# Performance work log

Hardware: AMD Instinct MI355X
Metric: run time of the kernel (lower is better)

## Reference

```python
import jax, jax.numpy as jnp
import numpy as np

TREND_SCALING = 0.6
DETAIL_PRESERVATION = 0.85
SPIKE_THRESHOLD = 3.5
SPIKE_DAMPING = 0.35
ITERATIONS = 2
EPS = 1e-6


def _smooth(x, kernel):
    # x: [B, C, L], kernel: [1, 1, W] (normalized box filter)
    W = kernel.shape[-1]
    pad = W // 2
    xp = jnp.pad(x, ((0, 0), (0, 0), (pad, pad)), mode='reflect')
    C = x.shape[1]
    w = jnp.broadcast_to(kernel, (C, 1, W))  # depthwise weight [C, 1, W]
    return jax.lax.conv_general_dilated(
        xp, w, window_strides=(1,), padding='VALID',
        dimension_numbers=('NCH', 'OIH', 'NCH'), feature_group_count=C)


def setup_inputs() -> dict:
    key = jax.random.key(0)
    x = jax.random.normal(key, (16, 32, 65536), dtype=jnp.float32)
    # buffers from __init__ with base_window=5
    detail_kernel = jnp.ones((1, 1, 5), dtype=jnp.float32) / 5.0
    trend_kernel = jnp.ones((1, 1, 11), dtype=jnp.float32) / 11.0
    return {"x": x, "detail_kernel": detail_kernel, "trend_kernel": trend_kernel}


def reference(x, detail_kernel, trend_kernel):
    current = x.astype(jnp.float32)
    for _ in range(ITERATIONS):
        trend = _smooth(current, trend_kernel)
        local = _smooth(current, detail_kernel)
        residual = current - local
        # torch .std uses Bessel's correction (ddof=1)
        scale = jnp.maximum(jnp.std(residual, axis=-1, keepdims=True, ddof=1), EPS)
        threshold = scale * SPIKE_THRESHOLD
        residual = jnp.where(jnp.abs(residual) > threshold,
                             residual * SPIKE_DAMPING, residual)
        residual = residual * DETAIL_PRESERVATION
        combined = (1.0 - TREND_SCALING) * local + TREND_SCALING * trend
        current = combined + residual
    return current
```

## Files before the change

kernel.cpp:

```cpp
#include <hip/hip_runtime.h>
#include <math.h>

#define LROW   65536
#define NROWS  512
#define CHUNK  4096
#define NCH    (LROW / CHUNK)
#define NT     256
#define EPT    (CHUNK / NT)
#define HALO   5
#define NELEM  (CHUNK + 2 * HALO)

#define TREND_SCALING       0.6f
#define DETAIL_PRESERVATION 0.85f
#define SPIKE_THRESHOLD     3.5f
#define SPIKE_DAMPING       0.35f
#define EPSV                1e-6f

#define PART_BYTES (NROWS * NCH * 2 * 8)

__device__ __forceinline__ int sw(int i) { return i + (i >> 4); }

template <bool STASH>
__global__ __launch_bounds__(NT) void k_sum(const float* __restrict__ src,
                                            const float* __restrict__ k5,
                                            double* __restrict__ partials,
                                            float* __restrict__ edges) {
    __shared__ float buf[NELEM + (NELEM >> 4) + 2];
    const int bid = blockIdx.x;
    const int row = bid >> 4;
    const int c = bid & (NCH - 1);
    const size_t rowBase = (size_t)row * LROW;
    const int cStart = c * CHUNK;
    const int tid = threadIdx.x;
    const float w5 = k5[0];

    const float4* src4 = (const float4*)(src + rowBase + cStart);
    for (int j4 = tid; j4 < CHUNK / 4; j4 += NT) {
        float4 t4 = src4[j4];
        int l = j4 * 4 + HALO;
        buf[sw(l)] = t4.x;
        buf[sw(l + 1)] = t4.y;
        buf[sw(l + 2)] = t4.z;
        buf[sw(l + 3)] = t4.w;
    }
    if (tid < 2 * HALO) {
        int j = (tid < HALO) ? tid : (CHUNK + tid);
        int g = cStart - HALO + j;
        g = (g < 0) ? -g : (g >= LROW ? 2 * LROW - 2 - g : g);
        buf[sw(j)] = src[rowBase + g];
    }
    __syncthreads();

    if (STASH && tid < 10) {
        int l = (tid < 5) ? (HALO + tid) : (CHUNK + tid - 5);
        edges[(size_t)bid * 10 + tid] = buf[sw(l)];
    }

    float v[EPT + 2 * HALO];
    const int base = tid * EPT;
#pragma unroll
    for (int j = 0; j < EPT + 2 * HALO; j++) v[j] = buf[sw(base + j)];

    double s = 0.0, q = 0.0;
#pragma unroll
    for (int k = 0; k < EPT; k++) {
        float lac = 0.f;
#pragma unroll
        for (int d = 0; d < 5; d++) lac = fmaf(v[k + 3 + d], w5, lac);
        float r = v[k + HALO] - lac;
        s += (double)r;
        q += (double)r * (double)r;
    }

    __shared__ double rs[NT], rq[NT];
    rs[tid] = s;
    rq[tid] = q;
    __syncthreads();
    for (int off = NT / 2; off > 0; off >>= 1) {
        if (tid < off) {
            rs[tid] += rs[tid + off];
            rq[tid] += rq[tid + off];
        }
        __syncthreads();
    }
    if (tid == 0) {
        partials[(size_t)bid * 2] = rs[0];
        partials[(size_t)bid * 2 + 1] = rq[0];
    }
}

__global__ void k_red(const double* __restrict__ partials, float* __restrict__ thr) {
    int r = blockIdx.x * blockDim.x + threadIdx.x;
    if (r >= NROWS) return;
    double s = 0.0, q = 0.0;
    for (int c = 0; c < NCH; c++) {
        s += partials[(size_t)(r * NCH + c) * 2];
        q += partials[(size_t)(r * NCH + c) * 2 + 1];
    }
    const double N = (double)LROW;
    double var = (q - s * s / N) / (N - 1.0);
    if (var < 0.0) var = 0.0;
    float sd = (float)sqrt(var);
    float scale = fmaxf(sd, EPSV);
    thr[r] = scale * SPIKE_THRESHOLD;
}

template <bool USE_EDGES>
__global__ __launch_bounds__(NT) void k_apply(const float* src, float* dst,
                                              const float* k5, const float* k11,
                                              const float* thr, const float* edges) {
    __shared__ float buf[NELEM + (NELEM >> 4) + 2];
    const int bid = blockIdx.x;
    const int row = bid >> 4;
    const int c = bid & (NCH - 1);
    const size_t rowBase = (size_t)row * LROW;
    const int cStart = c * CHUNK;
    const int tid = threadIdx.x;
    const float w5 = k5[0];
    const float w11 = k11[0];
    const float th = thr[row];

    const float4* src4 = (const float4*)(src + rowBase + cStart);
    for (int j4 = tid; j4 < CHUNK / 4; j4 += NT) {
        float4 t4 = src4[j4];
        int l = j4 * 4 + HALO;
        buf[sw(l)] = t4.x;
        buf[sw(l + 1)] = t4.y;
        buf[sw(l + 2)] = t4.z;
        buf[sw(l + 3)] = t4.w;
    }
    if (!USE_EDGES) {
        if (tid < 2 * HALO) {
            int j = (tid < HALO) ? tid : (CHUNK + tid);
            int g = cStart - HALO + j;
            g = (g < 0) ? -g : (g >= LROW ? 2 * LROW - 2 - g : g);
            buf[sw(j)] = src[rowBase + g];
        }
        __syncthreads();
    } else {
        __syncthreads();
        if (tid < HALO) {
            float val;
            if (c > 0)
                val = edges[((size_t)bid - 1) * 10 + 5 + tid];
            else
                val = buf[sw(10 - tid)];
            buf[sw(tid)] = val;
        } else if (tid < 2 * HALO) {
            int k = tid - HALO;
            float val;
            if (c < NCH - 1)
                val = edges[((size_t)bid + 1) * 10 + k];
            else
                val = buf[sw(CHUNK + 3 - k)];
            buf[sw(CHUNK + HALO + k)] = val;
        }
        __syncthreads();
    }

    float v[EPT + 2 * HALO];
    const int base = tid * EPT;
#pragma unroll
    for (int j = 0; j < EPT + 2 * HALO; j++) v[j] = buf[sw(base + j)];

    float o[EPT];
#pragma unroll
    for (int k = 0; k < EPT; k++) {
        float lac = 0.f, tac = 0.f;
#pragma unroll
        for (int d = 0; d < 5; d++) lac = fmaf(v[k + 3 + d], w5, lac);
#pragma unroll
        for (int d = 0; d < 11; d++) tac = fmaf(v[k + d], w11, tac);
        float cur = v[k + HALO];
        float r = cur - lac;
        r = (fabsf(r) > th) ? r * SPIKE_DAMPING : r;
        float comb = (1.0f - TREND_SCALING) * lac + TREND_SCALING * tac;
        o[k] = comb + DETAIL_PRESERVATION * r;
    }

    float4* dst4 = (float4*)(dst + rowBase + cStart + base);
#pragma unroll
    for (int k4 = 0; k4 < EPT / 4; k4++) {
        dst4[k4] = make_float4(o[4 * k4], o[4 * k4 + 1], o[4 * k4 + 2], o[4 * k4 + 3]);
    }
}

extern "C" void kernel_launch(void* const* d_in, const int* in_sizes, int n_in,
                              void* d_out, int out_size, void* d_ws, size_t ws_size,
                              hipStream_t stream) {
    const float* x = (const float*)d_in[0];
    const float* k5 = (const float*)d_in[1];
    const float* k11 = (const float*)d_in[2];
    float* out = (float*)d_out;
    char* ws = (char*)d_ws;
    double* partials = (double*)ws;
    float* thr = (float*)(ws + PART_BYTES);
    float* edges = (float*)(ws + PART_BYTES + 4096);

    dim3 grid(NROWS * NCH), block(NT);

    hipLaunchKernelGGL((k_sum<false>), grid, block, 0, stream, x, k5, partials, edges);
    hipLaunchKernelGGL(k_red, dim3(2), dim3(NT), 0, stream, partials, thr);
    hipLaunchKernelGGL((k_apply<false>), grid, block, 0, stream, x, out, k5, k11, thr, edges);

    hipLaunchKernelGGL((k_sum<true>), grid, block, 0, stream, out, k5, partials, edges);
    hipLaunchKernelGGL(k_red, dim3(2), dim3(NT), 0, stream, partials, thr);
    hipLaunchKernelGGL((k_apply<true>), grid, block, 0, stream, out, out, k5, k11, thr, edges);
}
```

Before: 363.0 us.

## Fuse both denoise iterations into one persistent kernel with one block per row

Replaces the six launches (sum, reduce and apply, each twice) with a single kernel in which each 512-thread block owns one row. The block walks the row in 8192-element chunks, loading the next chunk into registers while the current one is staged through shared memory. The row's std reduction is done in-block with wavefront shuffles, and the second, in-place iteration carries halos through shared memory. This removes launch gaps, the partials and edges round trips through global memory, and may let re-reads of a row hit in cache. In exchange the grid drops to 512 blocks with sequential chunk loops, so latency hiding depends on the one-chunk-ahead prefetch.

```diff
diff --git a/kernel.cpp b/kernel.cpp
--- a/kernel.cpp
+++ b/kernel.cpp
@@ -3,207 +3,167 @@
 
 #define LROW   65536
 #define NROWS  512
-#define CHUNK  4096
-#define NCH    (LROW / CHUNK)
-#define NT     256
-#define EPT    (CHUNK / NT)
+#define NT     512
+#define CK     8192
+#define NC     (LROW / CK)
+#define EPT    (CK / NT)
+#define V4     (CK / 4 / NT)
 #define HALO   5
-#define NELEM  (CHUNK + 2 * HALO)
+#define NEL    (CK + 2 * HALO)
 
 #define TREND_SCALING       0.6f
 #define DETAIL_PRESERVATION 0.85f
-#define SPIKE_THRESHOLD     3.5f
 #define SPIKE_DAMPING       0.35f
-#define EPSV                1e-6f
-
-#define PART_BYTES (NROWS * NCH * 2 * 8)
 
 __device__ __forceinline__ int sw(int i) { return i + (i >> 4); }
+__device__ __forceinline__ int refl(int g) {
+    return g < 0 ? -g : (g >= LROW ? 2 * LROW - 2 - g : g);
+}
 
-template <bool STASH>
-__global__ __launch_bounds__(NT) void k_sum(const float* __restrict__ src,
-                                            const float* __restrict__ k5,
-                                            double* __restrict__ partials,
-                                            float* __restrict__ edges) {
-    __shared__ float buf[NELEM + (NELEM >> 4) + 2];
-    const int bid = blockIdx.x;
-    const int row = bid >> 4;
-    const int c = bid & (NCH - 1);
-    const size_t rowBase = (size_t)row * LROW;
-    const int cStart = c * CHUNK;
-    const int tid = threadIdx.x;
-    const float w5 = k5[0];
+struct Pref { float4 m[V4]; float h; };
 
-    const float4* src4 = (const float4*)(src + rowBase + cStart);
-    for (int j4 = tid; j4 < CHUNK / 4; j4 += NT) {
-        float4 t4 = src4[j4];
-        int l = j4 * 4 + HALO;
-        buf[sw(l)] = t4.x;
-        buf[sw(l + 1)] = t4.y;
-        buf[sw(l + 2)] = t4.z;
-        buf[sw(l + 3)] = t4.w;
-    }
-    if (tid < 2 * HALO) {
-        int j = (tid < HALO) ? tid : (CHUNK + tid);
-        int g = cStart - HALO + j;
-        g = (g < 0) ? -g : (g >= LROW ? 2 * LROW - 2 - g : g);
-        buf[sw(j)] = src[rowBase + g];
-    }
-    __syncthreads();
-
-    if (STASH && tid < 10) {
-        int l = (tid < 5) ? (HALO + tid) : (CHUNK + tid - 5);
-        edges[(size_t)bid * 10 + tid] = buf[sw(l)];
-    }
-
-    float v[EPT + 2 * HALO];
-    const int base = tid * EPT;
+__device__ __forceinline__ void issue(const float* rowp, int c, int tid, Pref& p,
+                                      bool loadLeft) {
+    const float4* s4 = (const float4*)(rowp + c * CK);
 #pragma unroll
-    for (int j = 0; j < EPT + 2 * HALO; j++) v[j] = buf[sw(base + j)];
-
-    double s = 0.0, q = 0.0;
-#pragma unroll
-    for (int k = 0; k < EPT; k++) {
-        float lac = 0.f;
-#pragma unroll
-        for (int d = 0; d < 5; d++) lac = fmaf(v[k + 3 + d], w5, lac);
-        float r = v[k + HALO] - lac;
-        s += (double)r;
-        q += (double)r * (double)r;
-    }
-
-    __shared__ double rs[NT], rq[NT];
-    rs[tid] = s;
-    rq[tid] = q;
-    __syncthreads();
-    for (int off = NT / 2; off > 0; off >>= 1) {
-        if (tid < off) {
-            rs[tid] += rs[tid + off];
-            rq[tid] += rq[tid + off];
+    for (int i = 0; i < V4; i++) p.m[i] = s4[tid + i * NT];
+    if (tid < 10) {
+        if (tid >= 5 || loadLeft) {
+            int l = (tid < 5) ? tid : CK + tid;
+            int g = c * CK - HALO + l;
+            p.h = rowp[refl(g)];
         }
-        __syncthreads();
-    }
-    if (tid == 0) {
-        partials[(size_t)bid * 2] = rs[0];
-        partials[(size_t)bid * 2 + 1] = rq[0];
     }
 }
 
-__global__ void k_red(const double* __restrict__ partials, float* __restrict__ thr) {
-    int r = blockIdx.x * blockDim.x + threadIdx.x;
-    if (r >= NROWS) return;
-    double s = 0.0, q = 0.0;
-    for (int c = 0; c < NCH; c++) {
-        s += partials[(size_t)(r * NCH + c) * 2];
-        q += partials[(size_t)(r * NCH + c) * 2 + 1];
+__device__ __forceinline__ void stage(float* buf, int tid, const Pref& p,
+                                      const float* carryL, bool useCarry) {
+#pragma unroll
+    for (int i = 0; i < V4; i++) {
+        int l = (tid + i * NT) * 4 + HALO;
+        buf[sw(l)]     = p.m[i].x;
+        buf[sw(l + 1)] = p.m[i].y;
+        buf[sw(l + 2)] = p.m[i].z;
+        buf[sw(l + 3)] = p.m[i].w;
     }
-    const double N = (double)LROW;
-    double var = (q - s * s / N) / (N - 1.0);
-    if (var < 0.0) var = 0.0;
-    float sd = (float)sqrt(var);
-    float scale = fmaxf(sd, EPSV);
-    thr[r] = scale * SPIKE_THRESHOLD;
+    if (tid < 10) {
+        int l = (tid < 5) ? tid : CK + tid;
+        float v = (useCarry && tid < 5) ? carryL[tid] : p.h;
+        buf[sw(l)] = v;
+    }
 }
 
-template <bool USE_EDGES>
-__global__ __launch_bounds__(NT) void k_apply(const float* src, float* dst,
-                                              const float* k5, const float* k11,
-                                              const float* thr, const float* edges) {
-    __shared__ float buf[NELEM + (NELEM >> 4) + 2];
-    const int bid = blockIdx.x;
-    const int row = bid >> 4;
-    const int c = bid & (NCH - 1);
-    const size_t rowBase = (size_t)row * LROW;
-    const int cStart = c * CHUNK;
+__global__ __launch_bounds__(NT, 4) void fused_denoise(
+        const float* __restrict__ x, float* out,
+        const float* __restrict__ k5p, const float* __restrict__ k11p) {
+    __shared__ float  buf[NEL + (NEL >> 4) + 2];
+    __shared__ double red[(NT / 64) * 2];
+    __shared__ float  smThr;
+    __shared__ float  carry[8];
+
+    const int row = blockIdx.x;
     const int tid = threadIdx.x;
-    const float w5 = k5[0];
-    const float w11 = k11[0];
-    const float th = thr[row];
+    const float* xr  = x + (size_t)row * LROW;
+    float*       orow = out + (size_t)row * LROW;
+    const float w5  = k5p[0];
+    const float w11 = k11p[0];
 
-    const float4* src4 = (const float4*)(src + rowBase + cStart);
-    for (int j4 = tid; j4 < CHUNK / 4; j4 += NT) {
-        float4 t4 = src4[j4];
-        int l = j4 * 4 + HALO;
-        buf[sw(l)] = t4.x;
-        buf[sw(l + 1)] = t4.y;
-        buf[sw(l + 2)] = t4.z;
-        buf[sw(l + 3)] = t4.w;
-    }
-    if (!USE_EDGES) {
-        if (tid < 2 * HALO) {
-            int j = (tid < HALO) ? tid : (CHUNK + tid);
-            int g = cStart - HALO + j;
-            g = (g < 0) ? -g : (g >= LROW ? 2 * LROW - 2 - g : g);
-            buf[sw(j)] = src[rowBase + g];
+    auto sum_pass = [&](const float* src) -> float {
+        double s = 0.0, q = 0.0;
+        Pref pA, pB;
+        issue(src, 0, tid, pA, true);
+        for (int c = 0; c < NC; c++) {
+            Pref& cur = (c & 1) ? pB : pA;
+            Pref& nxt = (c & 1) ? pA : pB;
+            if (c + 1 < NC) issue(src, c + 1, tid, nxt, true);
+            __syncthreads();
+            stage(buf, tid, cur, nullptr, false);
+            __syncthreads();
+            float v[EPT + 2 * HALO];
+            const int base = tid * EPT;
+#pragma unroll
+            for (int j = 0; j < EPT + 2 * HALO; j++) v[j] = buf[sw(base + j)];
+#pragma unroll
+            for (int k = 0; k < EPT; k++) {
+                float lac = 0.f;
+#pragma unroll
+                for (int d = 0; d < 5; d++) lac = fmaf(v[k + 3 + d], w5, lac);
+                float r = v[k + HALO] - lac;
+                s += (double)r;
+                q += (double)r * (double)r;
+            }
+        }
+#pragma unroll
+        for (int off = 32; off > 0; off >>= 1) {
+            s += __shfl_down(s, off);
+            q += __shfl_down(q, off);
+        }
+        const int wid = tid >> 6, lane = tid & 63;
+        if (lane == 0) { red[2 * wid] = s; red[2 * wid + 1] = q; }
+        __syncthreads();
+        if (tid == 0) {
+            double S = 0.0, Q = 0.0;
+            for (int w = 0; w < NT / 64; w++) { S += red[2 * w]; Q += red[2 * w + 1]; }
+            const double N = (double)LROW;
+            double var = (Q - S * S / N) / (N - 1.0);
+            if (var < 0.0) var = 0.0;
+            smThr = fmaxf((float)sqrt(var), 1e-6f) * 3.5f;
         }
         __syncthreads();
-    } else {
-        __syncthreads();
-        if (tid < HALO) {
-            float val;
-            if (c > 0)
-                val = edges[((size_t)bid - 1) * 10 + 5 + tid];
-            else
-                val = buf[sw(10 - tid)];
-            buf[sw(tid)] = val;
-        } else if (tid < 2 * HALO) {
-            int k = tid - HALO;
-            float val;
-            if (c < NCH - 1)
-                val = edges[((size_t)bid + 1) * 10 + k];
-            else
-                val = buf[sw(CHUNK + 3 - k)];
-            buf[sw(CHUNK + HALO + k)] = val;
+        return smThr;
+    };
+
+    auto apply_pass = [&](const float* src, float th, bool inplace) {
+        Pref pA, pB;
+        issue(src, 0, tid, pA, true);
+        for (int c = 0; c < NC; c++) {
+            Pref& cur = (c & 1) ? pB : pA;
+            Pref& nxt = (c & 1) ? pA : pB;
+            if (c + 1 < NC) issue(src, c + 1, tid, nxt, !inplace);
+            __syncthreads();
+            stage(buf, tid, cur, carry, inplace && c > 0);
+            __syncthreads();
+            float v[EPT + 2 * HALO];
+            const int base = tid * EPT;
+#pragma unroll
+            for (int j = 0; j < EPT + 2 * HALO; j++) v[j] = buf[sw(base + j)];
+            if (inplace && tid < 5) carry[tid] = buf[sw(CK + tid)];
+            float o[EPT];
+#pragma unroll
+            for (int k = 0; k < EPT; k++) {
+                float lac = 0.f, tac = 0.f;
+#pragma unroll
+                for (int d = 0; d < 5; d++) lac = fmaf(v[k + 3 + d], w5, lac);
+#pragma unroll
+                for (int d = 0; d < 11; d++) tac = fmaf(v[k + d], w11, tac);
+                float cv = v[k + HALO];
+                float r = cv - lac;
+                r = (fabsf(r) > th) ? r * SPIKE_DAMPING : r;
+                o[k] = (1.0f - TREND_SCALING) * lac + TREND_SCALING * tac +
+                       DETAIL_PRESERVATION * r;
+            }
+            float4* d4 = (float4*)(orow + c * CK + tid * EPT);
+#pragma unroll
+            for (int k4 = 0; k4 < EPT / 4; k4++)
+                d4[k4] = make_float4(o[4 * k4], o[4 * k4 + 1],
+                                     o[4 * k4 + 2], o[4 * k4 + 3]);
         }
-        __syncthreads();
-    }
+    };
 
-    float v[EPT + 2 * HALO];
-    const int base = tid * EPT;
-#pragma unroll
-    for (int j = 0; j < EPT + 2 * HALO; j++) v[j] = buf[sw(base + j)];
-
-    float o[EPT];
-#pragma unroll
-    for (int k = 0; k < EPT; k++) {
-        float lac = 0.f, tac = 0.f;
-#pragma unroll
-        for (int d = 0; d < 5; d++) lac = fmaf(v[k + 3 + d], w5, lac);
-#pragma unroll
-        for (int d = 0; d < 11; d++) tac = fmaf(v[k + d], w11, tac);
-        float cur = v[k + HALO];
-        float r = cur - lac;
-        r = (fabsf(r) > th) ? r * SPIKE_DAMPING : r;
-        float comb = (1.0f - TREND_SCALING) * lac + TREND_SCALING * tac;
-        o[k] = comb + DETAIL_PRESERVATION * r;
-    }
-
-    float4* dst4 = (float4*)(dst + rowBase + cStart + base);
-#pragma unroll
-    for (int k4 = 0; k4 < EPT / 4; k4++) {
-        dst4[k4] = make_float4(o[4 * k4], o[4 * k4 + 1], o[4 * k4 + 2], o[4 * k4 + 3]);
-    }
+    float th1 = sum_pass(xr);
+    apply_pass(xr, th1, false);
+    __syncthreads();
+    float th2 = sum_pass(orow);
+    apply_pass(orow, th2, true);
 }
 
 extern "C" void kernel_launch(void* const* d_in, const int* in_sizes, int n_in,
                               void* d_out, int out_size, void* d_ws, size_t ws_size,
                               hipStream_t stream) {
-    const float* x = (const float*)d_in[0];
-    const float* k5 = (const float*)d_in[1];
+    const float* x   = (const float*)d_in[0];
+    const float* k5  = (const float*)d_in[1];
     const float* k11 = (const float*)d_in[2];
     float* out = (float*)d_out;
-    char* ws = (char*)d_ws;
-    double* partials = (double*)ws;
-    float* thr = (float*)(ws + PART_BYTES);
-    float* edges = (float*)(ws + PART_BYTES + 4096);
-
-    dim3 grid(NROWS * NCH), block(NT);
-
-    hipLaunchKernelGGL((k_sum<false>), grid, block, 0, stream, x, k5, partials, edges);
-    hipLaunchKernelGGL(k_red, dim3(2), dim3(NT), 0, stream, partials, thr);
-    hipLaunchKernelGGL((k_apply<false>), grid, block, 0, stream, x, out, k5, k11, thr, edges);
-
-    hipLaunchKernelGGL((k_sum<true>), grid, block, 0, stream, out, k5, partials, edges);
-    hipLaunchKernelGGL(k_red, dim3(2), dim3(NT), 0, stream, partials, thr);
-    hipLaunchKernelGGL((k_apply<true>), grid, block, 0, stream, out, out, k5, k11, thr, edges);
+    hipLaunchKernelGGL(fused_denoise, dim3(NROWS), dim3(NT), 0, stream,
+                       x, out, k5, k11);
 }
```

Result: slower. 540.6 us (+48.9%).
